# Kernel optimization log

Hardware: AMD Instinct MI355X
Metric: run time of the kernel (lower is better)

Reference implementation:

```python
import jax, jax.numpy as jnp
import numpy as np

NUM_EDGES = 10000
NUM_PATHS = 30000
MAX_LEN = 16
LINK_DIM = 128
PATH_DIM = 128


def setup_inputs() -> dict:
    key = jax.random.key(0)
    k0, k1, k2, k3, k4, k5, k6, k7 = jax.random.split(key, 8)
    inputs = jax.random.normal(k0, (NUM_EDGES, LINK_DIM), dtype=jnp.float32)
    # every path has exactly MAX_LEN hops -> unique (path, pos) scatter indices
    idx = jnp.repeat(jnp.arange(NUM_PATHS, dtype=jnp.int64), MAX_LEN)
    seqs = jnp.tile(jnp.arange(MAX_LEN, dtype=jnp.int64), NUM_PATHS)
    paths = jax.random.randint(k1, (NUM_PATHS * MAX_LEN,), 0, NUM_EDGES).astype(jnp.int64)
    # GRU params (Keras GRUCell, reset_after=True): kernel [D,3U], recurrent [U,3U], two bias rows
    s_in = 1.0 / np.sqrt(LINK_DIM)
    s_h = 1.0 / np.sqrt(PATH_DIM)
    kernel = jax.random.uniform(k2, (LINK_DIM, 3 * PATH_DIM), minval=-s_in, maxval=s_in, dtype=jnp.float32)
    rec_kernel = jax.random.uniform(k3, (PATH_DIM, 3 * PATH_DIM), minval=-s_h, maxval=s_h, dtype=jnp.float32)
    bias_i = jnp.zeros((3 * PATH_DIM,), dtype=jnp.float32)
    bias_r = jnp.zeros((3 * PATH_DIM,), dtype=jnp.float32)
    wq = jax.random.uniform(k4, (PATH_DIM, PATH_DIM), minval=-s_h, maxval=s_h, dtype=jnp.float32)
    wk = jax.random.uniform(k5, (PATH_DIM, PATH_DIM), minval=-s_h, maxval=s_h, dtype=jnp.float32)
    wv = jax.random.uniform(k6, (PATH_DIM, PATH_DIM), minval=-s_h, maxval=s_h, dtype=jnp.float32)
    return {"inputs": inputs, "paths": paths, "idx": idx, "seqs": seqs,
            "kernel": kernel, "rec_kernel": rec_kernel, "bias_i": bias_i, "bias_r": bias_r,
            "wq": wq, "wk": wk, "wv": wv}


def _gru_scan(link_inputs, kernel, rec_kernel, bias_i, bias_r):
    # link_inputs: [P, L, D] -> hidden_states [P, L, U], last_state [P, U]
    U = rec_kernel.shape[0]
    P = link_inputs.shape[0]
    xs = jnp.transpose(link_inputs, (1, 0, 2))  # [L, P, D]

    def step(h, x):
        xm = x @ kernel + bias_i          # [P, 3U]
        hm = h @ rec_kernel + bias_r      # [P, 3U]  (reset_after=True)
        xz, xr, xh = xm[:, :U], xm[:, U:2 * U], xm[:, 2 * U:]
        hz, hr, hh = hm[:, :U], hm[:, U:2 * U], hm[:, 2 * U:]
        z = jax.nn.sigmoid(xz + hz)
        r = jax.nn.sigmoid(xr + hr)
        cand = jnp.tanh(xh + r * hh)
        h_new = z * h + (1.0 - z) * cand
        return h_new, h_new

    h0 = jnp.zeros((P, U), dtype=link_inputs.dtype)
    last, hs = jax.lax.scan(step, h0, xs)
    return jnp.transpose(hs, (1, 0, 2)), last  # [P, L, U], [P, U]


def reference(inputs, paths, idx, seqs, kernel, rec_kernel, bias_i, bias_r, wq, wk, wv):
    h_tild = inputs[paths]  # gather: [P*L, D]
    link_inputs = jnp.zeros((NUM_PATHS, MAX_LEN, LINK_DIM), dtype=inputs.dtype)
    link_inputs = link_inputs.at[idx, seqs].set(h_tild)  # scatter_nd
    hidden_states, last_state = _gru_scan(link_inputs, kernel, rec_kernel, bias_i, bias_r)
    key = jnp.einsum('plu,uv->plv', hidden_states, wk)
    query = last_state @ wq                     # [P, U]
    value = jnp.einsum('plu,uv->plv', hidden_states, wv)
    att = jnp.einsum('plv,pv->pl', key, query)  # raw scores, no softmax (faithful)
    context = jnp.einsum('pl,plv->pv', att, value)[:, None, :]  # [P, 1, U]
    return context
```

## Files before the change

### kernel.cpp

```cpp
#include <hip/hip_runtime.h>
#include <hip/hip_bf16.h>


#define NUM_PATHS 30000
#define T_PATHS 32
#define NTILES ((NUM_PATHS + T_PATHS - 1) / T_PATHS)

typedef float f32x4 __attribute__((ext_vector_type(4)));
typedef short bf16x8 __attribute__((ext_vector_type(8)));

__device__ __forceinline__ short f2bf(float f) {
    union { float f; unsigned u; } v; v.f = f;
    return (short)((v.u + 0x8000u) >> 16);
}
__device__ __forceinline__ float bf2f(short s) {
    union { unsigned u; float f; } v; v.u = ((unsigned)(unsigned short)s) << 16;
    return v.f;
}
__device__ __forceinline__ float fsig(float x) {
    return __builtin_amdgcn_rcpf(1.0f + __expf(-x));
}
__device__ __forceinline__ float ftanh(float x) {
    return 1.0f - 2.0f * __builtin_amdgcn_rcpf(1.0f + __expf(2.0f * x));
}

__global__ void wqk_kernel(const float* __restrict__ wq, const float* __restrict__ wk,
                           float* __restrict__ Wqk) {
    int id = blockIdx.x * 256 + threadIdx.x;
    int u = id >> 7, i = id & 127;
    float s = 0.f;
    #pragma unroll 8
    for (int v = 0; v < 128; ++v) s += wq[u * 128 + v] * wk[i * 128 + v];
    Wqk[u * 128 + i] = s;
}

#define PACK_THREADS 12288
#define CONV_CHUNKS 160000
__global__ void prep_kernel(const float* __restrict__ inputs,
                            const float* __restrict__ Wx, const float* __restrict__ Wr,
                            short* __restrict__ tab, short* __restrict__ wpk) {
    int id = blockIdx.x * 256 + threadIdx.x;
    if (id < PACK_THREADS) {
        int f = id >> 9, rem = id & 511;
        int w = rem >> 6, lane = rem & 63;
        int quad = lane >> 4, c16 = lane & 15;
        int col = 16 * w + c16;
        short o[8];
        #pragma unroll
        for (int j = 0; j < 8; ++j) {
            float v;
            if (f < 16) {
                int k = (f & 7) * 32 + quad * 8 + j;
                int cc = col + ((f < 8) ? 0 : 128);
                v = (k < 128) ? Wx[k * 384 + cc] : Wr[(k - 128) * 384 + cc];
            } else {
                int k = ((f - 16) & 3) * 32 + quad * 8 + j;
                v = (f < 20) ? Wx[k * 384 + 256 + col] : Wr[k * 384 + 256 + col];
            }
            o[j] = f2bf(v);
        }
        *(bf16x8*)&wpk[id * 8] = *(bf16x8*)o;
    }
    int cid = id - PACK_THREADS;
    if (cid >= 0 && cid < CONV_CHUNKS) {
        float4 a = *(const float4*)&inputs[cid * 8];
        float4 b = *(const float4*)&inputs[cid * 8 + 4];
        short o[8] = {f2bf(a.x), f2bf(a.y), f2bf(a.z), f2bf(a.w),
                      f2bf(b.x), f2bf(b.y), f2bf(b.z), f2bf(b.w)};
        *(bf16x8*)&tab[cid * 8] = *(bf16x8*)o;
    }
}

#define MFMA(a, b, c) __builtin_amdgcn_mfma_f32_16x16x32_bf16((a), (b), (c), 0, 0, 0)

#define ROWS 136
#define HSLOT 4360
#define XROWS (T_PATHS * ROWS)

__global__ __launch_bounds__(512, 2) void path_emb_kernel(
    const short* __restrict__ tab, const int* __restrict__ paths,
    const short* __restrict__ wpk,
    const float* __restrict__ bias_i, const float* __restrict__ bias_r,
    const float* __restrict__ Wqk, const float* __restrict__ wv,
    float* __restrict__ out)
{
    __shared__ __align__(16) short s_hist[16][HSLOT];
    __shared__ __align__(16) short s_xb[2][XROWS];
    __shared__ float s_att[T_PATHS][20];
    short* const s_ea = s_xb[0];
    short* const s_eb = s_xb[1];

    const int tid  = threadIdx.x;
    const int w    = tid >> 6;
    const int lane = tid & 63;
    const int quad = lane >> 4;
    const int c16  = lane & 15;
    const int ucol = 16 * w + c16;
    const int srow = tid >> 4;
    const int schunk = (tid & 15) * 8;

    const float bz  = bias_i[ucol] + bias_r[ucol];
    const float brr = bias_i[128 + ucol] + bias_r[128 + ucol];
    const float bxh = bias_i[256 + ucol];
    const float bhh = bias_r[256 + ucol];

    bf16x8 Ball[24];
    #pragma unroll
    for (int f = 0; f < 24; ++f)
        Ball[f] = *(const bf16x8*)&wpk[((f * 8 + w) * 64 + lane) * 8];

    for (int tile = blockIdx.x; tile < NTILES; tile += gridDim.x) {
        const int p0 = tile * T_PATHS;
        const int spr = min(p0 + srow, NUM_PATHS - 1) * 16;

        __syncthreads();
        {
            int e = paths[spr];
            *(bf16x8*)&s_xb[0][srow * ROWS + schunk] = *(const bf16x8*)&tab[e * 128 + schunk];
        }

        float hreg[8];
        #pragma unroll
        for (int i = 0; i < 8; ++i) hreg[i] = 0.f;

        for (int t = 0; t < 16; ++t) {
            __syncthreads();

            if (t < 15) {
                int e = paths[spr + t + 1];
                *(bf16x8*)&s_xb[(t + 1) & 1][srow * ROWS + schunk] =
                    *(const bf16x8*)&tab[e * 128 + schunk];
            }

            bf16x8 ax[2][4], ah[2][4];
            #pragma unroll
            for (int mt = 0; mt < 2; ++mt)
                #pragma unroll
                for (int kc = 0; kc < 4; ++kc)
                    ax[mt][kc] = *(const bf16x8*)&s_xb[t & 1][(mt * 16 + c16) * ROWS + kc * 32 + quad * 8];
            if (t > 0) {
                #pragma unroll
                for (int mt = 0; mt < 2; ++mt)
                    #pragma unroll
                    for (int kc = 0; kc < 4; ++kc)
                        ah[mt][kc] = *(const bf16x8*)&s_hist[t - 1][(mt * 16 + c16) * ROWS + kc * 32 + quad * 8];
            }

            f32x4 az[2], ar[2], acx[2], ach[2];
            #pragma unroll
            for (int mt = 0; mt < 2; ++mt) {
                az[mt]  = (f32x4){bz, bz, bz, bz};
                ar[mt]  = (f32x4){brr, brr, brr, brr};
                acx[mt] = (f32x4){bxh, bxh, bxh, bxh};
                ach[mt] = (f32x4){bhh, bhh, bhh, bhh};
            }
            #pragma unroll
            for (int mt = 0; mt < 2; ++mt)
                #pragma unroll
                for (int kc = 0; kc < 4; ++kc) {
                    az[mt]  = MFMA(ax[mt][kc], Ball[kc],      az[mt]);
                    ar[mt]  = MFMA(ax[mt][kc], Ball[8 + kc],  ar[mt]);
                    acx[mt] = MFMA(ax[mt][kc], Ball[16 + kc], acx[mt]);
                }
            if (t > 0) {
                #pragma unroll
                for (int mt = 0; mt < 2; ++mt)
                    #pragma unroll
                    for (int kc = 0; kc < 4; ++kc) {
                        az[mt]  = MFMA(ah[mt][kc], Ball[4 + kc],  az[mt]);
                        ar[mt]  = MFMA(ah[mt][kc], Ball[12 + kc], ar[mt]);
                        ach[mt] = MFMA(ah[mt][kc], Ball[20 + kc], ach[mt]);
                    }
            }

            #pragma unroll
            for (int mt = 0; mt < 2; ++mt)
                #pragma unroll
                for (int r = 0; r < 4; ++r) {
                    int i = mt * 4 + r;
                    float z    = fsig(az[mt][r]);
                    float rr   = fsig(ar[mt][r]);
                    float cand = ftanh(acx[mt][r] + rr * ach[mt][r]);
                    hreg[i] = cand + z * (hreg[i] - cand);
                    s_hist[t][(mt * 16 + quad * 4 + r) * ROWS + ucol] = f2bf(hreg[i]);
                }
        }

        #pragma unroll
        for (int mt = 0; mt < 2; ++mt)
            #pragma unroll
            for (int r = 0; r < 4; ++r) {
                float hf = hreg[mt * 4 + r];
                short hi = f2bf(hf);
                s_ea[(mt * 16 + quad * 4 + r) * ROWS + ucol] = f2bf(hf - bf2f(hi));
            }
        __syncthreads();

        f32x4 uacc[2];
        { f32x4 zz = {0.f, 0.f, 0.f, 0.f}; uacc[0] = zz; uacc[1] = zz; }
        #pragma unroll
        for (int kc = 0; kc < 4; ++kc) {
            bf16x8 bhi, blo;
            #pragma unroll
            for (int j = 0; j < 8; ++j) {
                float v = Wqk[(kc * 32 + quad * 8 + j) * 128 + ucol];
                short h = f2bf(v);
                bhi[j] = h; blo[j] = f2bf(v - bf2f(h));
            }
            #pragma unroll
            for (int mt = 0; mt < 2; ++mt) {
                bf16x8 Ahi = *(const bf16x8*)&s_hist[15][(mt * 16 + c16) * ROWS + kc * 32 + quad * 8];
                bf16x8 Alo = *(const bf16x8*)&s_ea[(mt * 16 + c16) * ROWS + kc * 32 + quad * 8];
                uacc[mt] = MFMA(Ahi, bhi, uacc[mt]);
                uacc[mt] = MFMA(Ahi, blo, uacc[mt]);
                uacc[mt] = MFMA(Alo, bhi, uacc[mt]);
            }
        }
        __syncthreads();

        #pragma unroll
        for (int mt = 0; mt < 2; ++mt)
            #pragma unroll
            for (int r = 0; r < 4; ++r) {
                float v = uacc[mt][r];
                short hi = f2bf(v);
                int off = (mt * 16 + quad * 4 + r) * ROWS + ucol;
                s_ea[off] = hi;
                s_eb[off] = f2bf(v - bf2f(hi));
            }
        __syncthreads();

        {
            int p = tid >> 4, l = tid & 15;
            const short* uh = &s_ea[p * ROWS];
            const short* ul = &s_eb[p * ROWS];
            const short* hh = &s_hist[l][p * ROWS];
            float a = 0.f;
            #pragma unroll
            for (int u8 = 0; u8 < 128; u8 += 8) {
                bf16x8 vh = *(const bf16x8*)&uh[u8];
                bf16x8 vl = *(const bf16x8*)&ul[u8];
                bf16x8 vt = *(const bf16x8*)&hh[u8];
                #pragma unroll
                for (int j = 0; j < 8; ++j)
                    a += (bf2f(vh[j]) + bf2f(vl[j])) * bf2f(vt[j]);
            }
            s_att[p][l] = a;
        }
        __syncthreads();

        {
            int p = tid >> 4, v0 = (tid & 15) * 8;
            float ctx[8];
            #pragma unroll
            for (int j = 0; j < 8; ++j) ctx[j] = 0.f;
            #pragma unroll
            for (int l = 0; l < 16; ++l) {
                float al = s_att[p][l];
                bf16x8 hv = *(const bf16x8*)&s_hist[l][p * ROWS + v0];
                #pragma unroll
                for (int j = 0; j < 8; ++j) ctx[j] += al * bf2f(hv[j]);
            }
            #pragma unroll
            for (int j = 0; j < 8; ++j) {
                short hi = f2bf(ctx[j]);
                s_ea[p * ROWS + v0 + j] = hi;
                s_eb[p * ROWS + v0 + j] = f2bf(ctx[j] - bf2f(hi));
            }
        }
        __syncthreads();

        f32x4 oacc[2];
        { f32x4 zz = {0.f, 0.f, 0.f, 0.f}; oacc[0] = zz; oacc[1] = zz; }
        #pragma unroll
        for (int kc = 0; kc < 4; ++kc) {
            bf16x8 bhi, blo;
            #pragma unroll
            for (int j = 0; j < 8; ++j) {
                float v = wv[(kc * 32 + quad * 8 + j) * 128 + ucol];
                short h = f2bf(v);
                bhi[j] = h; blo[j] = f2bf(v - bf2f(h));
            }
            #pragma unroll
            for (int mt = 0; mt < 2; ++mt) {
                bf16x8 Ahi = *(const bf16x8*)&s_ea[(mt * 16 + c16) * ROWS + kc * 32 + quad * 8];
                bf16x8 Alo = *(const bf16x8*)&s_eb[(mt * 16 + c16) * ROWS + kc * 32 + quad * 8];
                oacc[mt] = MFMA(Ahi, bhi, oacc[mt]);
                oacc[mt] = MFMA(Ahi, blo, oacc[mt]);
                oacc[mt] = MFMA(Alo, bhi, oacc[mt]);
            }
        }
        #pragma unroll
        for (int mt = 0; mt < 2; ++mt)
            #pragma unroll
            for (int r = 0; r < 4; ++r) {
                int prow = p0 + mt * 16 + quad * 4 + r;
                if (prow < NUM_PATHS) out[prow * 128 + ucol] = oacc[mt][r];
            }
    }
}

extern "C" void kernel_launch(void* const* d_in, const int* in_sizes, int n_in,
                              void* d_out, int out_size, void* d_ws, size_t ws_size,
                              hipStream_t stream) {
    const float* inputs = (const float*)d_in[0];
    const int*   paths  = (const int*)d_in[1];
    const float* wx  = (const float*)d_in[4];
    const float* wr  = (const float*)d_in[5];
    const float* bi  = (const float*)d_in[6];
    const float* br  = (const float*)d_in[7];
    const float* wq  = (const float*)d_in[8];
    const float* wk  = (const float*)d_in[9];
    const float* wvp = (const float*)d_in[10];

    char* ws = (char*)d_ws;
    float* Wqk = (float*)ws;
    short* tab = (short*)(ws + 65536);
    short* wpk = (short*)(ws + 65536 + 2560000);

    wqk_kernel<<<64, 256, 0, stream>>>(wq, wk, Wqk);
    prep_kernel<<<(PACK_THREADS + CONV_CHUNKS + 255) / 256, 256, 0, stream>>>(
        inputs, wx, wr, tab, wpk);
    path_emb_kernel<<<256, 512, 0, stream>>>(tab, paths, wpk, bi, br, Wqk, wvp,
                                             (float*)d_out);
}
```

Measured before the change: 236.5 us.

## Process two independent 16-path tiles per block and prepack Wqk/Wv weights

The path kernel now handles a pair of 16-path tiles per block iteration. The two tiles' GRU MFMA chains are interleaved, which shortens the dependency chains and halves the shared history footprint per tile. The Wq·Wk product and the Wv hi/lo bf16 split are computed once in the prep kernel into the packed weight buffer, replacing per-tile conversion from fp32 global loads. One launch is also dropped. The last pair duplicates tile 1874 for padding, so it writes the same rows twice with identical values.

Result: faster. 223.4 us (-5.6%).

```diff
diff --git a/kernel.cpp b/kernel.cpp
--- a/kernel.cpp
+++ b/kernel.cpp
@@ -1,10 +1,10 @@
 #include <hip/hip_runtime.h>
-#include <hip/hip_bf16.h>
 
 
 #define NUM_PATHS 30000
-#define T_PATHS 32
-#define NTILES ((NUM_PATHS + T_PATHS - 1) / T_PATHS)
+#define T 16
+#define NTILES 1875
+#define NPAIRS 938
 
 typedef float f32x4 __attribute__((ext_vector_type(4)));
 typedef short bf16x8 __attribute__((ext_vector_type(8)));
@@ -20,27 +20,21 @@
 __device__ __forceinline__ float fsig(float x) {
     return __builtin_amdgcn_rcpf(1.0f + __expf(-x));
 }
-__device__ __forceinline__ float ftanh(float x) {
+__device__ __forceinline__ float ftanhf_(float x) {
     return 1.0f - 2.0f * __builtin_amdgcn_rcpf(1.0f + __expf(2.0f * x));
 }
 
-__global__ void wqk_kernel(const float* __restrict__ wq, const float* __restrict__ wk,
-                           float* __restrict__ Wqk) {
-    int id = blockIdx.x * 256 + threadIdx.x;
-    int u = id >> 7, i = id & 127;
-    float s = 0.f;
-    #pragma unroll 8
-    for (int v = 0; v < 128; ++v) s += wq[u * 128 + v] * wk[i * 128 + v];
-    Wqk[u * 128 + i] = s;
-}
-
-#define PACK_THREADS 12288
-#define CONV_CHUNKS 160000
+#define GRU_T 12288
+#define QK_T 16384
+#define WV_T 2048
+#define TAB_C 160000
 __global__ void prep_kernel(const float* __restrict__ inputs,
                             const float* __restrict__ Wx, const float* __restrict__ Wr,
+                            const float* __restrict__ wq, const float* __restrict__ wk,
+                            const float* __restrict__ wv,
                             short* __restrict__ tab, short* __restrict__ wpk) {
     int id = blockIdx.x * 256 + threadIdx.x;
-    if (id < PACK_THREADS) {
+    if (id < GRU_T) {
         int f = id >> 9, rem = id & 511;
         int w = rem >> 6, lane = rem & 63;
         int quad = lane >> 4, c16 = lane & 15;
@@ -60,9 +54,40 @@
             o[j] = f2bf(v);
         }
         *(bf16x8*)&wpk[id * 8] = *(bf16x8*)o;
-    }
-    int cid = id - PACK_THREADS;
-    if (cid >= 0 && cid < CONV_CHUNKS) {
+        return;
+    }
+    if (id < GRU_T + QK_T) {
+        int t2 = id - GRU_T;
+        int j = t2 & 7, lane = (t2 >> 3) & 63, w = (t2 >> 9) & 7, kc = t2 >> 12;
+        int quad = lane >> 4, c16 = lane & 15, col = 16 * w + c16;
+        int k = kc * 32 + quad * 8 + j;
+        const float* qr = wq + k * 128;
+        const float* kr = wk + col * 128;
+        float s = 0.f;
+        #pragma unroll 8
+        for (int vv = 0; vv < 128; ++vv) s += qr[vv] * kr[vv];
+        short hi = f2bf(s);
+        wpk[(((24 + kc) * 8 + w) * 64 + lane) * 8 + j] = hi;
+        wpk[(((28 + kc) * 8 + w) * 64 + lane) * 8 + j] = f2bf(s - bf2f(hi));
+        return;
+    }
+    if (id < GRU_T + QK_T + WV_T) {
+        int t2 = id - GRU_T - QK_T;
+        int lane = t2 & 63, w = (t2 >> 6) & 7, kc = t2 >> 9;
+        int quad = lane >> 4, c16 = lane & 15, col = 16 * w + c16;
+        short hi8[8], lo8[8];
+        #pragma unroll
+        for (int j = 0; j < 8; ++j) {
+            float v = wv[(kc * 32 + quad * 8 + j) * 128 + col];
+            hi8[j] = f2bf(v);
+            lo8[j] = f2bf(v - bf2f(hi8[j]));
+        }
+        *(bf16x8*)&wpk[(((32 + kc) * 8 + w) * 64 + lane) * 8] = *(bf16x8*)hi8;
+        *(bf16x8*)&wpk[(((36 + kc) * 8 + w) * 64 + lane) * 8] = *(bf16x8*)lo8;
+        return;
+    }
+    int cid = id - (GRU_T + QK_T + WV_T);
+    if (cid < TAB_C) {
         float4 a = *(const float4*)&inputs[cid * 8];
         float4 b = *(const float4*)&inputs[cid * 8 + 4];
         short o[8] = {f2bf(a.x), f2bf(a.y), f2bf(a.z), f2bf(a.w),
@@ -74,21 +99,17 @@
 #define MFMA(a, b, c) __builtin_amdgcn_mfma_f32_16x16x32_bf16((a), (b), (c), 0, 0, 0)
 
 #define ROWS 136
-#define HSLOT 4360
-#define XROWS (T_PATHS * ROWS)
+#define HSLOT 2184
 
 __global__ __launch_bounds__(512, 2) void path_emb_kernel(
     const short* __restrict__ tab, const int* __restrict__ paths,
     const short* __restrict__ wpk,
     const float* __restrict__ bias_i, const float* __restrict__ bias_r,
-    const float* __restrict__ Wqk, const float* __restrict__ wv,
     float* __restrict__ out)
 {
-    __shared__ __align__(16) short s_hist[16][HSLOT];
-    __shared__ __align__(16) short s_xb[2][XROWS];
-    __shared__ float s_att[T_PATHS][20];
-    short* const s_ea = s_xb[0];
-    short* const s_eb = s_xb[1];
+    __shared__ __align__(16) short s_hist[2][16][HSLOT];
+    __shared__ __align__(16) short s_xb[2][2][T * ROWS];
+    __shared__ float s_att[2][16][20];
 
     const int tid  = threadIdx.x;
     const int w    = tid >> 6;
@@ -96,8 +117,10 @@
     const int quad = lane >> 4;
     const int c16  = lane & 15;
     const int ucol = 16 * w + c16;
-    const int srow = tid >> 4;
-    const int schunk = (tid & 15) * 8;
+    const int st   = tid >> 8;
+    const int rid  = tid & 255;
+    const int srow = rid >> 4;
+    const int schunk = (rid & 15) * 8;
 
     const float bz  = bias_i[ucol] + bias_r[ucol];
     const float brr = bias_i[128 + ucol] + bias_r[128 + ucol];
@@ -109,132 +132,125 @@
     for (int f = 0; f < 24; ++f)
         Ball[f] = *(const bf16x8*)&wpk[((f * 8 + w) * 64 + lane) * 8];
 
-    for (int tile = blockIdx.x; tile < NTILES; tile += gridDim.x) {
-        const int p0 = tile * T_PATHS;
-        const int spr = min(p0 + srow, NUM_PATHS - 1) * 16;
+    for (int pi = blockIdx.x; pi < NPAIRS; pi += gridDim.x) {
+        const int tA = 2 * pi;
+        const int tB = (2 * pi + 1 < NTILES) ? 2 * pi + 1 : NTILES - 1;
+        const int p0A = tA * T, p0B = tB * T;
+        const int spr = ((st ? p0B : p0A) + srow) * 16;
 
         __syncthreads();
         {
             int e = paths[spr];
-            *(bf16x8*)&s_xb[0][srow * ROWS + schunk] = *(const bf16x8*)&tab[e * 128 + schunk];
-        }
-
-        float hreg[8];
-        #pragma unroll
-        for (int i = 0; i < 8; ++i) hreg[i] = 0.f;
+            *(bf16x8*)&s_xb[st][0][srow * ROWS + schunk] = *(const bf16x8*)&tab[e * 128 + schunk];
+        }
+
+        float hA[4] = {0.f, 0.f, 0.f, 0.f}, hB[4] = {0.f, 0.f, 0.f, 0.f};
 
         for (int t = 0; t < 16; ++t) {
             __syncthreads();
 
             if (t < 15) {
                 int e = paths[spr + t + 1];
-                *(bf16x8*)&s_xb[(t + 1) & 1][srow * ROWS + schunk] =
+                *(bf16x8*)&s_xb[st][(t + 1) & 1][srow * ROWS + schunk] =
                     *(const bf16x8*)&tab[e * 128 + schunk];
             }
 
-            bf16x8 ax[2][4], ah[2][4];
-            #pragma unroll
-            for (int mt = 0; mt < 2; ++mt)
-                #pragma unroll
-                for (int kc = 0; kc < 4; ++kc)
-                    ax[mt][kc] = *(const bf16x8*)&s_xb[t & 1][(mt * 16 + c16) * ROWS + kc * 32 + quad * 8];
+            bf16x8 axA[4], axB[4], ahA[4], ahB[4];
+            #pragma unroll
+            for (int kc = 0; kc < 4; ++kc) {
+                axA[kc] = *(const bf16x8*)&s_xb[0][t & 1][c16 * ROWS + kc * 32 + quad * 8];
+                axB[kc] = *(const bf16x8*)&s_xb[1][t & 1][c16 * ROWS + kc * 32 + quad * 8];
+            }
             if (t > 0) {
                 #pragma unroll
-                for (int mt = 0; mt < 2; ++mt)
-                    #pragma unroll
-                    for (int kc = 0; kc < 4; ++kc)
-                        ah[mt][kc] = *(const bf16x8*)&s_hist[t - 1][(mt * 16 + c16) * ROWS + kc * 32 + quad * 8];
-            }
-
-            f32x4 az[2], ar[2], acx[2], ach[2];
-            #pragma unroll
-            for (int mt = 0; mt < 2; ++mt) {
-                az[mt]  = (f32x4){bz, bz, bz, bz};
-                ar[mt]  = (f32x4){brr, brr, brr, brr};
-                acx[mt] = (f32x4){bxh, bxh, bxh, bxh};
-                ach[mt] = (f32x4){bhh, bhh, bhh, bhh};
-            }
-            #pragma unroll
-            for (int mt = 0; mt < 2; ++mt)
+                for (int kc = 0; kc < 4; ++kc) {
+                    ahA[kc] = *(const bf16x8*)&s_hist[0][t - 1][c16 * ROWS + kc * 32 + quad * 8];
+                    ahB[kc] = *(const bf16x8*)&s_hist[1][t - 1][c16 * ROWS + kc * 32 + quad * 8];
+                }
+            }
+
+            f32x4 azA = {bz, bz, bz, bz},    azB = azA;
+            f32x4 arA = {brr, brr, brr, brr}, arB = arA;
+            f32x4 acxA = {bxh, bxh, bxh, bxh}, acxB = acxA;
+            f32x4 achA = {bhh, bhh, bhh, bhh}, achB = achA;
+
+            #pragma unroll
+            for (int kc = 0; kc < 4; ++kc) {
+                azA  = MFMA(axA[kc], Ball[kc],      azA);
+                azB  = MFMA(axB[kc], Ball[kc],      azB);
+                arA  = MFMA(axA[kc], Ball[8 + kc],  arA);
+                arB  = MFMA(axB[kc], Ball[8 + kc],  arB);
+                acxA = MFMA(axA[kc], Ball[16 + kc], acxA);
+                acxB = MFMA(axB[kc], Ball[16 + kc], acxB);
+            }
+            if (t > 0) {
                 #pragma unroll
                 for (int kc = 0; kc < 4; ++kc) {
-                    az[mt]  = MFMA(ax[mt][kc], Ball[kc],      az[mt]);
-                    ar[mt]  = MFMA(ax[mt][kc], Ball[8 + kc],  ar[mt]);
-                    acx[mt] = MFMA(ax[mt][kc], Ball[16 + kc], acx[mt]);
+                    azA  = MFMA(ahA[kc], Ball[4 + kc],  azA);
+                    azB  = MFMA(ahB[kc], Ball[4 + kc],  azB);
+                    arA  = MFMA(ahA[kc], Ball[12 + kc], arA);
+                    arB  = MFMA(ahB[kc], Ball[12 + kc], arB);
+                    achA = MFMA(ahA[kc], Ball[20 + kc], achA);
+                    achB = MFMA(ahB[kc], Ball[20 + kc], achB);
                 }
-            if (t > 0) {
-                #pragma unroll
-                for (int mt = 0; mt < 2; ++mt)
-                    #pragma unroll
-                    for (int kc = 0; kc < 4; ++kc) {
-                        az[mt]  = MFMA(ah[mt][kc], Ball[4 + kc],  az[mt]);
-                        ar[mt]  = MFMA(ah[mt][kc], Ball[12 + kc], ar[mt]);
-                        ach[mt] = MFMA(ah[mt][kc], Ball[20 + kc], ach[mt]);
-                    }
-            }
-
-            #pragma unroll
-            for (int mt = 0; mt < 2; ++mt)
-                #pragma unroll
-                for (int r = 0; r < 4; ++r) {
-                    int i = mt * 4 + r;
-                    float z    = fsig(az[mt][r]);
-                    float rr   = fsig(ar[mt][r]);
-                    float cand = ftanh(acx[mt][r] + rr * ach[mt][r]);
-                    hreg[i] = cand + z * (hreg[i] - cand);
-                    s_hist[t][(mt * 16 + quad * 4 + r) * ROWS + ucol] = f2bf(hreg[i]);
-                }
-        }
-
-        #pragma unroll
-        for (int mt = 0; mt < 2; ++mt)
+            }
+
             #pragma unroll
             for (int r = 0; r < 4; ++r) {
-                float hf = hreg[mt * 4 + r];
-                short hi = f2bf(hf);
-                s_ea[(mt * 16 + quad * 4 + r) * ROWS + ucol] = f2bf(hf - bf2f(hi));
-            }
-        __syncthreads();
-
-        f32x4 uacc[2];
-        { f32x4 zz = {0.f, 0.f, 0.f, 0.f}; uacc[0] = zz; uacc[1] = zz; }
+                float z    = fsig(azA[r]);
+                float rr   = fsig(arA[r]);
+                float cand = ftanhf_(acxA[r] + rr * achA[r]);
+                hA[r] = cand + z * (hA[r] - cand);
+                s_hist[0][t][(quad * 4 + r) * ROWS + ucol] = f2bf(hA[r]);
+            }
+            #pragma unroll
+            for (int r = 0; r < 4; ++r) {
+                float z    = fsig(azB[r]);
+                float rr   = fsig(arB[r]);
+                float cand = ftanhf_(acxB[r] + rr * achB[r]);
+                hB[r] = cand + z * (hB[r] - cand);
+                s_hist[1][t][(quad * 4 + r) * ROWS + ucol] = f2bf(hB[r]);
+            }
+        }
+
+        #pragma unroll
+        for (int r = 0; r < 4; ++r) {
+            float hf = hA[r]; short hi = f2bf(hf);
+            s_xb[0][0][(quad * 4 + r) * ROWS + ucol] = f2bf(hf - bf2f(hi));
+            hf = hB[r]; hi = f2bf(hf);
+            s_xb[1][0][(quad * 4 + r) * ROWS + ucol] = f2bf(hf - bf2f(hi));
+        }
+        __syncthreads();
+
+        f32x4 uA = {0.f, 0.f, 0.f, 0.f}, uB = uA;
         #pragma unroll
         for (int kc = 0; kc < 4; ++kc) {
-            bf16x8 bhi, blo;
-            #pragma unroll
-            for (int j = 0; j < 8; ++j) {
-                float v = Wqk[(kc * 32 + quad * 8 + j) * 128 + ucol];
-                short h = f2bf(v);
-                bhi[j] = h; blo[j] = f2bf(v - bf2f(h));
-            }
-            #pragma unroll
-            for (int mt = 0; mt < 2; ++mt) {
-                bf16x8 Ahi = *(const bf16x8*)&s_hist[15][(mt * 16 + c16) * ROWS + kc * 32 + quad * 8];
-                bf16x8 Alo = *(const bf16x8*)&s_ea[(mt * 16 + c16) * ROWS + kc * 32 + quad * 8];
-                uacc[mt] = MFMA(Ahi, bhi, uacc[mt]);
-                uacc[mt] = MFMA(Ahi, blo, uacc[mt]);
-                uacc[mt] = MFMA(Alo, bhi, uacc[mt]);
-            }
-        }
-        __syncthreads();
-
-        #pragma unroll
-        for (int mt = 0; mt < 2; ++mt)
-            #pragma unroll
-            for (int r = 0; r < 4; ++r) {
-                float v = uacc[mt][r];
-                short hi = f2bf(v);
-                int off = (mt * 16 + quad * 4 + r) * ROWS + ucol;
-                s_ea[off] = hi;
-                s_eb[off] = f2bf(v - bf2f(hi));
-            }
+            bf16x8 bqh = *(const bf16x8*)&wpk[(((24 + kc) * 8 + w) * 64 + lane) * 8];
+            bf16x8 bql = *(const bf16x8*)&wpk[(((28 + kc) * 8 + w) * 64 + lane) * 8];
+            bf16x8 AhA = *(const bf16x8*)&s_hist[0][15][c16 * ROWS + kc * 32 + quad * 8];
+            bf16x8 AlA = *(const bf16x8*)&s_xb[0][0][c16 * ROWS + kc * 32 + quad * 8];
+            bf16x8 AhB = *(const bf16x8*)&s_hist[1][15][c16 * ROWS + kc * 32 + quad * 8];
+            bf16x8 AlB = *(const bf16x8*)&s_xb[1][0][c16 * ROWS + kc * 32 + quad * 8];
+            uA = MFMA(AhA, bqh, uA); uA = MFMA(AhA, bql, uA); uA = MFMA(AlA, bqh, uA);
+            uB = MFMA(AhB, bqh, uB); uB = MFMA(AhB, bql, uB); uB = MFMA(AlB, bqh, uB);
+        }
+        __syncthreads();
+
+        #pragma unroll
+        for (int r = 0; r < 4; ++r) {
+            int off = (quad * 4 + r) * ROWS + ucol;
+            float v = uA[r]; short hi = f2bf(v);
+            s_xb[0][0][off] = hi; s_xb[0][1][off] = f2bf(v - bf2f(hi));
+            v = uB[r]; hi = f2bf(v);
+            s_xb[1][0][off] = hi; s_xb[1][1][off] = f2bf(v - bf2f(hi));
+        }
         __syncthreads();
 
         {
-            int p = tid >> 4, l = tid & 15;
-            const short* uh = &s_ea[p * ROWS];
-            const short* ul = &s_eb[p * ROWS];
-            const short* hh = &s_hist[l][p * ROWS];
+            int et = tid >> 8, p = (tid >> 4) & 15, l = tid & 15;
+            const short* uh = &s_xb[et][0][p * ROWS];
+            const short* ul = &s_xb[et][1][p * ROWS];
+            const short* hh = &s_hist[et][l][p * ROWS];
             float a = 0.f;
             #pragma unroll
             for (int u8 = 0; u8 < 128; u8 += 8) {
@@ -245,58 +261,48 @@
                 for (int j = 0; j < 8; ++j)
                     a += (bf2f(vh[j]) + bf2f(vl[j])) * bf2f(vt[j]);
             }
-            s_att[p][l] = a;
+            s_att[et][p][l] = a;
         }
         __syncthreads();
 
         {
-            int p = tid >> 4, v0 = (tid & 15) * 8;
+            int et = tid >> 8, p = (tid >> 4) & 15, v0 = (tid & 15) * 8;
             float ctx[8];
             #pragma unroll
             for (int j = 0; j < 8; ++j) ctx[j] = 0.f;
             #pragma unroll
             for (int l = 0; l < 16; ++l) {
-                float al = s_att[p][l];
-                bf16x8 hv = *(const bf16x8*)&s_hist[l][p * ROWS + v0];
+                float al = s_att[et][p][l];
+                bf16x8 hv = *(const bf16x8*)&s_hist[et][l][p * ROWS + v0];
                 #pragma unroll
                 for (int j = 0; j < 8; ++j) ctx[j] += al * bf2f(hv[j]);
             }
             #pragma unroll
             for (int j = 0; j < 8; ++j) {
                 short hi = f2bf(ctx[j]);
-                s_ea[p * ROWS + v0 + j] = hi;
-                s_eb[p * ROWS + v0 + j] = f2bf(ctx[j] - bf2f(hi));
-            }
-        }
-        __syncthreads();
-
-        f32x4 oacc[2];
-        { f32x4 zz = {0.f, 0.f, 0.f, 0.f}; oacc[0] = zz; oacc[1] = zz; }
+                s_xb[et][0][p * ROWS + v0 + j] = hi;
+                s_xb[et][1][p * ROWS + v0 + j] = f2bf(ctx[j] - bf2f(hi));
+            }
+        }
+        __syncthreads();
+
+        f32x4 oA = {0.f, 0.f, 0.f, 0.f}, oB = oA;
         #pragma unroll
         for (int kc = 0; kc < 4; ++kc) {
-            bf16x8 bhi, blo;
-            #pragma unroll
-            for (int j = 0; j < 8; ++j) {
-                float v = wv[(kc * 32 + quad * 8 + j) * 128 + ucol];
-                short h = f2bf(v);
-                bhi[j] = h; blo[j] = f2bf(v - bf2f(h));
-            }
-            #pragma unroll
-            for (int mt = 0; mt < 2; ++mt) {
-                bf16x8 Ahi = *(const bf16x8*)&s_ea[(mt * 16 + c16) * ROWS + kc * 32 + quad * 8];
-                bf16x8 Alo = *(const bf16x8*)&s_eb[(mt * 16 + c16) * ROWS + kc * 32 + quad * 8];
-                oacc[mt] = MFMA(Ahi, bhi, oacc[mt]);
-                oacc[mt] = MFMA(Ahi, blo, oacc[mt]);
-                oacc[mt] = MFMA(Alo, bhi, oacc[mt]);
-            }
-        }
-        #pragma unroll
-        for (int mt = 0; mt < 2; ++mt)
-            #pragma unroll
-            for (int r = 0; r < 4; ++r) {
-                int prow = p0 + mt * 16 + quad * 4 + r;
-                if (prow < NUM_PATHS) out[prow * 128 + ucol] = oacc[mt][r];
-            }
+            bf16x8 bwh = *(const bf16x8*)&wpk[(((32 + kc) * 8 + w) * 64 + lane) * 8];
+            bf16x8 bwl = *(const bf16x8*)&wpk[(((36 + kc) * 8 + w) * 64 + lane) * 8];
+            bf16x8 AhA = *(const bf16x8*)&s_xb[0][0][c16 * ROWS + kc * 32 + quad * 8];
+            bf16x8 AlA = *(const bf16x8*)&s_xb[0][1][c16 * ROWS + kc * 32 + quad * 8];
+            bf16x8 AhB = *(const bf16x8*)&s_xb[1][0][c16 * ROWS + kc * 32 + quad * 8];
+            bf16x8 AlB = *(const bf16x8*)&s_xb[1][1][c16 * ROWS + kc * 32 + quad * 8];
+            oA = MFMA(AhA, bwh, oA); oA = MFMA(AhA, bwl, oA); oA = MFMA(AlA, bwh, oA);
+            oB = MFMA(AhB, bwh, oB); oB = MFMA(AhB, bwl, oB); oB = MFMA(AlB, bwh, oB);
+        }
+        #pragma unroll
+        for (int r = 0; r < 4; ++r) {
+            out[(p0A + quad * 4 + r) * 128 + ucol] = oA[r];
+            out[(p0B + quad * 4 + r) * 128 + ucol] = oB[r];
+        }
     }
 }
 
@@ -314,13 +320,11 @@
     const float* wvp = (const float*)d_in[10];
 
     char* ws = (char*)d_ws;
-    float* Wqk = (float*)ws;
-    short* tab = (short*)(ws + 65536);
-    short* wpk = (short*)(ws + 65536 + 2560000);
-
-    wqk_kernel<<<64, 256, 0, stream>>>(wq, wk, Wqk);
-    prep_kernel<<<(PACK_THREADS + CONV_CHUNKS + 255) / 256, 256, 0, stream>>>(
-        inputs, wx, wr, tab, wpk);
-    path_emb_kernel<<<256, 512, 0, stream>>>(tab, paths, wpk, bi, br, Wqk, wvp,
-                                             (float*)d_out);
-}
+    short* tab = (short*)ws;
+    short* wpk = (short*)(ws + 2560000);
+
+    int prep_n = GRU_T + QK_T + WV_T + TAB_C;
+    prep_kernel<<<(prep_n + 255) / 256, 256, 0, stream>>>(
+        inputs, wx, wr, wq, wk, wvp, tab, wpk);
+    path_emb_kernel<<<256, 512, 0, stream>>>(tab, paths, wpk, bi, br, (float*)d_out);
+}
```
